# Optimization experiments

Hardware: AMD Instinct MI355X
Metric: run time of the kernel (lower is better)

The kernel has to match this reference:

```python
import jax, jax.numpy as jnp
import numpy as np

N, NTIMES, D_FEAT = 2048, 32, 128


def setup_inputs() -> dict:
    key = jax.random.key(0)
    k1, k2 = jax.random.split(key)
    return {
        "target_fairness": jnp.zeros((), dtype=jnp.float32),
        "prediction": jax.random.uniform(k1, (N, NTIMES), dtype=jnp.float32),
        "X_distance": jax.random.normal(k2, (N, D_FEAT), dtype=jnp.float32),
        "ntimes": NTIMES,
        "scale": jnp.ones((), dtype=jnp.float32),
    }


def reference(target_fairness, prediction, X_distance, ntimes, scale):
    n = prediction.shape[0]
    # cosine distance matrix: 1 - cos_sim, matches sklearn cosine_distances
    norms = jnp.linalg.norm(X_distance, axis=1, keepdims=True)
    Xn = X_distance / norms
    dist = 1.0 - Xn @ Xn.T  # [N, N]
    # pairwise |pred_j - pred_k| over all time points: [N, N, T]
    diff = jnp.abs(prediction[:, None, :] - prediction[None, :, :])
    hinge = jnp.maximum(0.0, diff - scale * dist[:, :, None])
    # only pairs k > j contribute
    mask = jnp.triu(jnp.ones((n, n), dtype=bool), k=1)
    R_beta = jnp.sum(jnp.where(mask[:, :, None], hinge, 0.0))
    model_fairness = 2.0 * R_beta / (n * (n - 1) * ntimes)
    return jnp.maximum(0.0, model_fairness - target_fairness)
```

## Files before the change

### kernel.cpp

```cpp
#include <hip/hip_runtime.h>

#define N 2048
#define T 32
#define D 128
#define BT 32
#define MT (N / BT)
#define NTILES (MT * (MT + 1) / 2)
#define STR 36

typedef float floatx4 __attribute__((ext_vector_type(4)));
typedef short bf16x8 __attribute__((ext_vector_type(8)));

#define LGKM0() __builtin_amdgcn_s_waitcnt(0xc07f)

__device__ __forceinline__ void split8(float4 a, float4 b, bf16x8& h, bf16x8& l) {
  float v[8] = {a.x, a.y, a.z, a.w, b.x, b.y, b.z, b.w};
#pragma unroll
  for (int i = 0; i < 8; ++i) {
    unsigned u = __float_as_uint(v[i]);
    h[i] = (short)(u >> 16);
    float lo = v[i] - __uint_as_float(u & 0xffff0000u);
    l[i] = (short)(__float_as_uint(lo) >> 16);
  }
}

__device__ __forceinline__ float sumsq8(float4 a, float4 b) {
  return a.x * a.x + a.y * a.y + a.z * a.z + a.w * a.w +
         b.x * b.x + b.y * b.y + b.z * b.z + b.w * b.w;
}

__global__ __launch_bounds__(64) void pair_kernel(
    const float* __restrict__ pred,
    const float* __restrict__ X,
    const float* __restrict__ scale_p,
    double* __restrict__ partials) {
  __shared__ float Pa[BT * STR], Pb[BT * STR];
  __shared__ float nrmA[BT], nrmB[BT];

  const int t = blockIdx.x;
  int a = (int)((2 * MT + 1 -
                 sqrtf((float)((2 * MT + 1) * (2 * MT + 1) - 8 * t))) * 0.5f);
  while (a > 0 && t < a * MT - a * (a - 1) / 2) --a;
  while (t >= (a + 1) * MT - (a + 1) * a / 2) ++a;
  const int b = a + (t - (a * MT - a * (a - 1) / 2));

  const int tid  = threadIdx.x;
  const int m    = tid & 15;
  const int quad = tid >> 4;
  const int aRow0 = a * BT, bRow0 = b * BT;
  const float scale = scale_p[0];

  {
    const int srow = tid >> 1, co = (tid & 1) << 4;
    const float* par = pred + (size_t)(aRow0 + srow) * T + co;
    const float* pbr = pred + (size_t)(bRow0 + srow) * T + co;
#pragma unroll
    for (int j = 0; j < 4; ++j) {
      *(float4*)(&Pa[srow * STR + co + 4 * j]) = *(const float4*)(par + 4 * j);
      *(float4*)(&Pb[srow * STR + co + 4 * j]) = *(const float4*)(pbr + 4 * j);
    }
  }

  floatx4 acc[2][2];
#pragma unroll
  for (int I = 0; I < 2; ++I)
#pragma unroll
    for (int J = 0; J < 2; ++J) acc[I][J] = (floatx4){0.f, 0.f, 0.f, 0.f};
  float ssA[2] = {0.f, 0.f}, ssB[2] = {0.f, 0.f};

  const float* xa0 = X + (size_t)(aRow0 + m) * D + quad * 8;
  const float* xb0 = X + (size_t)(bRow0 + m) * D + quad * 8;

#pragma unroll
  for (int ks = 0; ks < 4; ++ks) {
    bf16x8 hA[2], lA[2], hB[2], lB[2];
#pragma unroll
    for (int I = 0; I < 2; ++I) {
      float4 u0 = *(const float4*)(xa0 + (size_t)I * 16 * D + ks * 32);
      float4 u1 = *(const float4*)(xa0 + (size_t)I * 16 * D + ks * 32 + 4);
      ssA[I] += sumsq8(u0, u1);
      split8(u0, u1, hA[I], lA[I]);
      float4 w0 = *(const float4*)(xb0 + (size_t)I * 16 * D + ks * 32);
      float4 w1 = *(const float4*)(xb0 + (size_t)I * 16 * D + ks * 32 + 4);
      ssB[I] += sumsq8(w0, w1);
      split8(w0, w1, hB[I], lB[I]);
    }
#pragma unroll
    for (int I = 0; I < 2; ++I)
#pragma unroll
      for (int J = 0; J < 2; ++J) {
        acc[I][J] = __builtin_amdgcn_mfma_f32_16x16x32_bf16(hA[I], hB[J],
                                                            acc[I][J], 0, 0, 0);
        acc[I][J] = __builtin_amdgcn_mfma_f32_16x16x32_bf16(hA[I], lB[J],
                                                            acc[I][J], 0, 0, 0);
        acc[I][J] = __builtin_amdgcn_mfma_f32_16x16x32_bf16(lA[I], hB[J],
                                                            acc[I][J], 0, 0, 0);
      }
  }

#pragma unroll
  for (int I = 0; I < 2; ++I) {
    ssA[I] += __shfl_xor(ssA[I], 16, 64);
    ssA[I] += __shfl_xor(ssA[I], 32, 64);
    ssB[I] += __shfl_xor(ssB[I], 16, 64);
    ssB[I] += __shfl_xor(ssB[I], 32, 64);
  }
  if (quad == 0) {
#pragma unroll
    for (int I = 0; I < 2; ++I) {
      nrmA[16 * I + m] = rsqrtf(ssA[I]);
      nrmB[16 * I + m] = rsqrtf(ssB[I]);
    }
  }
  LGKM0();

  float na[2][4], nb[2];
#pragma unroll
  for (int I = 0; I < 2; ++I) {
#pragma unroll
    for (int r = 0; r < 4; ++r) na[I][r] = nrmA[16 * I + quad * 4 + r];
    nb[I] = nrmB[16 * I + m];
  }
  float sd[2][2][4], ps[2][2][4];
#pragma unroll
  for (int I = 0; I < 2; ++I)
#pragma unroll
    for (int J = 0; J < 2; ++J)
#pragma unroll
      for (int r = 0; r < 4; ++r) {
        sd[I][J][r] = scale * (1.0f - acc[I][J][r] * na[I][r] * nb[J]);
        ps[I][J][r] = 0.0f;
      }

#pragma unroll
  for (int t4 = 0; t4 < 8; ++t4) {
    float4 qb[2];
    qb[0] = *(const float4*)(&Pb[m * STR + t4 * 4]);
    qb[1] = *(const float4*)(&Pb[(16 + m) * STR + t4 * 4]);
#pragma unroll
    for (int I = 0; I < 2; ++I)
#pragma unroll
      for (int r = 0; r < 4; ++r) {
        float4 qa = *(const float4*)(&Pa[(16 * I + quad * 4 + r) * STR + t4 * 4]);
#pragma unroll
        for (int J = 0; J < 2; ++J) {
          float s = sd[I][J][r];
          ps[I][J][r] += fmaxf(fabsf(qa.x - qb[J].x), s) +
                         fmaxf(fabsf(qa.y - qb[J].y), s) +
                         fmaxf(fabsf(qa.z - qb[J].z), s) +
                         fmaxf(fabsf(qa.w - qb[J].w), s);
        }
      }
  }

  float tsum = 0.0f;
#pragma unroll
  for (int I = 0; I < 2; ++I)
#pragma unroll
    for (int J = 0; J < 2; ++J)
#pragma unroll
      for (int r = 0; r < 4; ++r) {
        int j = aRow0 + 16 * I + quad * 4 + r;
        int k = bRow0 + 16 * J + m;
        tsum += (k > j) ? (ps[I][J][r] - 32.0f * sd[I][J][r]) : 0.0f;
      }

  double dsum = (double)tsum;
#pragma unroll
  for (int off = 32; off > 0; off >>= 1) dsum += __shfl_down(dsum, off, 64);
  if (tid == 0) partials[blockIdx.x] = dsum;
}

__global__ __launch_bounds__(256) void finalize_kernel(
    const double* __restrict__ partials, const float* __restrict__ target,
    float* __restrict__ out) {
  __shared__ double red[4];
  double s = 0.0;
  for (int i = threadIdx.x; i < NTILES; i += 256) s += partials[i];
#pragma unroll
  for (int off = 32; off > 0; off >>= 1) s += __shfl_down(s, off, 64);
  int wave = threadIdx.x >> 6, lane = threadIdx.x & 63;
  if (lane == 0) red[wave] = s;
  __syncthreads();
  if (threadIdx.x == 0) {
    double tot = red[0] + red[1] + red[2] + red[3];
    double mf  = 2.0 * tot / ((double)N * (double)(N - 1) * (double)T);
    double r   = mf - (double)target[0];
    out[0] = (float)(r > 0.0 ? r : 0.0);
  }
}

extern "C" void kernel_launch(void* const* d_in, const int* in_sizes, int n_in,
                              void* d_out, int out_size, void* d_ws, size_t ws_size,
                              hipStream_t stream) {
  const float* target = (const float*)d_in[0];
  const float* pred   = (const float*)d_in[1];
  const float* X      = (const float*)d_in[2];
  const float* scale  = (const float*)d_in[4];

  double* partials = (double*)d_ws;

  pair_kernel<<<dim3(NTILES), dim3(64), 0, stream>>>(pred, X, scale, partials);
  finalize_kernel<<<dim3(1), dim3(256), 0, stream>>>(partials, target,
                                                     (float*)d_out);
}
```

Before: 88.09 us.

## Split fused pair kernel into gram and hinge kernels with time-split tiles

```diff
diff --git a/kernel.cpp b/kernel.cpp
--- a/kernel.cpp
+++ b/kernel.cpp
@@ -6,7 +6,7 @@
 #define BT 32
 #define MT (N / BT)
 #define NTILES (MT * (MT + 1) / 2)
-#define STR 36
+#define PSTR 20
 
 typedef float floatx4 __attribute__((ext_vector_type(4)));
 typedef short bf16x8 __attribute__((ext_vector_type(8)));
@@ -29,37 +29,28 @@
          b.x * b.x + b.y * b.y + b.z * b.z + b.w * b.w;
 }
 
-__global__ __launch_bounds__(64) void pair_kernel(
-    const float* __restrict__ pred,
+__device__ __forceinline__ void tile_decode(int t, int& a, int& b) {
+  a = (int)((2 * MT + 1 -
+             sqrtf((float)((2 * MT + 1) * (2 * MT + 1) - 8 * t))) * 0.5f);
+  while (a > 0 && t < a * MT - a * (a - 1) / 2) --a;
+  while (t >= (a + 1) * MT - (a + 1) * a / 2) ++a;
+  b = a + (t - (a * MT - a * (a - 1) / 2));
+}
+
+__global__ __launch_bounds__(64) void gram_kernel(
     const float* __restrict__ X,
     const float* __restrict__ scale_p,
-    double* __restrict__ partials) {
-  __shared__ float Pa[BT * STR], Pb[BT * STR];
+    float* __restrict__ sd_out) {
   __shared__ float nrmA[BT], nrmB[BT];
 
-  const int t = blockIdx.x;
-  int a = (int)((2 * MT + 1 -
-                 sqrtf((float)((2 * MT + 1) * (2 * MT + 1) - 8 * t))) * 0.5f);
-  while (a > 0 && t < a * MT - a * (a - 1) / 2) --a;
-  while (t >= (a + 1) * MT - (a + 1) * a / 2) ++a;
-  const int b = a + (t - (a * MT - a * (a - 1) / 2));
+  int a, b;
+  tile_decode(blockIdx.x, a, b);
 
   const int tid  = threadIdx.x;
   const int m    = tid & 15;
   const int quad = tid >> 4;
   const int aRow0 = a * BT, bRow0 = b * BT;
   const float scale = scale_p[0];
-
-  {
-    const int srow = tid >> 1, co = (tid & 1) << 4;
-    const float* par = pred + (size_t)(aRow0 + srow) * T + co;
-    const float* pbr = pred + (size_t)(bRow0 + srow) * T + co;
-#pragma unroll
-    for (int j = 0; j < 4; ++j) {
-      *(float4*)(&Pa[srow * STR + co + 4 * j]) = *(const float4*)(par + 4 * j);
-      *(float4*)(&Pb[srow * STR + co + 4 * j]) = *(const float4*)(pbr + 4 * j);
-    }
-  }
 
   floatx4 acc[2][2];
 #pragma unroll
@@ -121,6 +112,44 @@
     for (int r = 0; r < 4; ++r) na[I][r] = nrmA[16 * I + quad * 4 + r];
     nb[I] = nrmB[16 * I + m];
   }
+  float* out = sd_out + (size_t)blockIdx.x * 1024 + tid;
+#pragma unroll
+  for (int I = 0; I < 2; ++I)
+#pragma unroll
+    for (int J = 0; J < 2; ++J)
+#pragma unroll
+      for (int r = 0; r < 4; ++r)
+        out[(I * 8 + J * 4 + r) * 64] =
+            scale * (1.0f - acc[I][J][r] * na[I][r] * nb[J]);
+}
+
+__global__ __launch_bounds__(64) void hinge_kernel(
+    const float* __restrict__ pred,
+    const float* __restrict__ sd_in,
+    double* __restrict__ partials) {
+  __shared__ float Pa[BT * PSTR], Pb[BT * PSTR];
+
+  const int tile = blockIdx.x >> 1;
+  const int th   = blockIdx.x & 1;
+  int a, b;
+  tile_decode(tile, a, b);
+
+  const int tid  = threadIdx.x;
+  const int m    = tid & 15;
+  const int quad = tid >> 4;
+  const int aRow0 = a * BT, bRow0 = b * BT;
+
+  {
+    const int srow = tid >> 1, co = (tid & 1) << 3;
+    const float* par = pred + (size_t)(aRow0 + srow) * T + th * 16 + co;
+    const float* pbr = pred + (size_t)(bRow0 + srow) * T + th * 16 + co;
+    *(float4*)(&Pa[srow * PSTR + co])     = *(const float4*)(par);
+    *(float4*)(&Pa[srow * PSTR + co + 4]) = *(const float4*)(par + 4);
+    *(float4*)(&Pb[srow * PSTR + co])     = *(const float4*)(pbr);
+    *(float4*)(&Pb[srow * PSTR + co + 4]) = *(const float4*)(pbr + 4);
+  }
+
+  const float* sin_ = sd_in + (size_t)tile * 1024 + tid;
   float sd[2][2][4], ps[2][2][4];
 #pragma unroll
   for (int I = 0; I < 2; ++I)
@@ -128,20 +157,21 @@
     for (int J = 0; J < 2; ++J)
 #pragma unroll
       for (int r = 0; r < 4; ++r) {
-        sd[I][J][r] = scale * (1.0f - acc[I][J][r] * na[I][r] * nb[J]);
+        sd[I][J][r] = sin_[(I * 8 + J * 4 + r) * 64];
         ps[I][J][r] = 0.0f;
       }
-
-#pragma unroll
-  for (int t4 = 0; t4 < 8; ++t4) {
+  LGKM0();
+
+#pragma unroll
+  for (int t4 = 0; t4 < 4; ++t4) {
     float4 qb[2];
-    qb[0] = *(const float4*)(&Pb[m * STR + t4 * 4]);
-    qb[1] = *(const float4*)(&Pb[(16 + m) * STR + t4 * 4]);
+    qb[0] = *(const float4*)(&Pb[m * PSTR + t4 * 4]);
+    qb[1] = *(const float4*)(&Pb[(16 + m) * PSTR + t4 * 4]);
 #pragma unroll
     for (int I = 0; I < 2; ++I)
 #pragma unroll
       for (int r = 0; r < 4; ++r) {
-        float4 qa = *(const float4*)(&Pa[(16 * I + quad * 4 + r) * STR + t4 * 4]);
+        float4 qa = *(const float4*)(&Pa[(16 * I + quad * 4 + r) * PSTR + t4 * 4]);
 #pragma unroll
         for (int J = 0; J < 2; ++J) {
           float s = sd[I][J][r];
@@ -162,7 +192,7 @@
       for (int r = 0; r < 4; ++r) {
         int j = aRow0 + 16 * I + quad * 4 + r;
         int k = bRow0 + 16 * J + m;
-        tsum += (k > j) ? (ps[I][J][r] - 32.0f * sd[I][J][r]) : 0.0f;
+        tsum += (k > j) ? (ps[I][J][r] - 16.0f * sd[I][J][r]) : 0.0f;
       }
 
   double dsum = (double)tsum;
@@ -176,7 +206,7 @@
     float* __restrict__ out) {
   __shared__ double red[4];
   double s = 0.0;
-  for (int i = threadIdx.x; i < NTILES; i += 256) s += partials[i];
+  for (int i = threadIdx.x; i < 2 * NTILES; i += 256) s += partials[i];
 #pragma unroll
   for (int off = 32; off > 0; off >>= 1) s += __shfl_down(s, off, 64);
   int wave = threadIdx.x >> 6, lane = threadIdx.x & 63;
@@ -198,9 +228,11 @@
   const float* X      = (const float*)d_in[2];
   const float* scale  = (const float*)d_in[4];
 
-  double* partials = (double*)d_ws;
-
-  pair_kernel<<<dim3(NTILES), dim3(64), 0, stream>>>(pred, X, scale, partials);
+  float*  sd       = (float*)d_ws;
+  double* partials = (double*)((char*)d_ws + (16u << 20));
+
+  gram_kernel<<<dim3(NTILES), dim3(64), 0, stream>>>(X, scale, sd);
+  hinge_kernel<<<dim3(2 * NTILES), dim3(64), 0, stream>>>(pred, sd, partials);
   finalize_kernel<<<dim3(1), dim3(256), 0, stream>>>(partials, target,
                                                      (float*)d_out);
 }
```

Result: slower. 91.41 us (+3.8%).

## Split fused pair kernel into presplit, Gram-matrix, and hinge kernels

Applied to the files above, without the earlier changes.

```diff
diff --git a/kernel.cpp b/kernel.cpp
--- a/kernel.cpp
+++ b/kernel.cpp
@@ -6,43 +6,44 @@
 #define BT 32
 #define MT (N / BT)
 #define NTILES (MT * (MT + 1) / 2)
-#define STR 36
+#define HJ 8
+#define NHBLK 4224
 
 typedef float floatx4 __attribute__((ext_vector_type(4)));
 typedef short bf16x8 __attribute__((ext_vector_type(8)));
 
-#define LGKM0() __builtin_amdgcn_s_waitcnt(0xc07f)
-
-__device__ __forceinline__ void split8(float4 a, float4 b, bf16x8& h, bf16x8& l) {
-  float v[8] = {a.x, a.y, a.z, a.w, b.x, b.y, b.z, b.w};
-#pragma unroll
-  for (int i = 0; i < 8; ++i) {
-    unsigned u = __float_as_uint(v[i]);
-    h[i] = (short)(u >> 16);
-    float lo = v[i] - __uint_as_float(u & 0xffff0000u);
-    l[i] = (short)(__float_as_uint(lo) >> 16);
-  }
+__device__ __forceinline__ void tile_decode(int t, int& a, int& b) {
+  a = (int)((2 * MT + 1 -
+             sqrtf((float)((2 * MT + 1) * (2 * MT + 1) - 8 * t))) * 0.5f);
+  while (a > 0 && t < a * MT - a * (a - 1) / 2) --a;
+  while (t >= (a + 1) * MT - (a + 1) * a / 2) ++a;
+  b = a + (t - (a * MT - a * (a - 1) / 2));
 }
 
-__device__ __forceinline__ float sumsq8(float4 a, float4 b) {
-  return a.x * a.x + a.y * a.y + a.z * a.z + a.w * a.w +
-         b.x * b.x + b.y * b.y + b.z * b.z + b.w * b.w;
+__global__ __launch_bounds__(256) void presplit_kernel(
+    const float* __restrict__ X, unsigned* __restrict__ hX,
+    unsigned* __restrict__ lX) {
+  const int row  = blockIdx.x * 4 + (threadIdx.x >> 6);
+  const int lane = threadIdx.x & 63;
+  float2 v = ((const float2*)(X + (size_t)row * D))[lane];
+  float ss = v.x * v.x + v.y * v.y;
+#pragma unroll
+  for (int off = 32; off > 0; off >>= 1) ss += __shfl_xor(ss, off, 64);
+  const float rn = rsqrtf(ss);
+  const float ax = v.x * rn, ay = v.y * rn;
+  const unsigned ux = __float_as_uint(ax), uy = __float_as_uint(ay);
+  const float lxf = ax - __uint_as_float(ux & 0xffff0000u);
+  const float lyf = ay - __uint_as_float(uy & 0xffff0000u);
+  hX[(size_t)row * 64 + lane] = (ux >> 16) | ((uy >> 16) << 16);
+  lX[(size_t)row * 64 + lane] =
+      (__float_as_uint(lxf) >> 16) | ((__float_as_uint(lyf) >> 16) << 16);
 }
 
-__global__ __launch_bounds__(64) void pair_kernel(
-    const float* __restrict__ pred,
-    const float* __restrict__ X,
-    const float* __restrict__ scale_p,
-    double* __restrict__ partials) {
-  __shared__ float Pa[BT * STR], Pb[BT * STR];
-  __shared__ float nrmA[BT], nrmB[BT];
-
-  const int t = blockIdx.x;
-  int a = (int)((2 * MT + 1 -
-                 sqrtf((float)((2 * MT + 1) * (2 * MT + 1) - 8 * t))) * 0.5f);
-  while (a > 0 && t < a * MT - a * (a - 1) / 2) --a;
-  while (t >= (a + 1) * MT - (a + 1) * a / 2) ++a;
-  const int b = a + (t - (a * MT - a * (a - 1) / 2));
+__global__ __launch_bounds__(64) void gram_kernel(
+    const unsigned short* __restrict__ hX, const unsigned short* __restrict__ lX,
+    const float* __restrict__ scale_p, float* __restrict__ sdm) {
+  int a, b;
+  tile_decode(blockIdx.x, a, b);
 
   const int tid  = threadIdx.x;
   const int m    = tid & 15;
@@ -50,40 +51,26 @@
   const int aRow0 = a * BT, bRow0 = b * BT;
   const float scale = scale_p[0];
 
-  {
-    const int srow = tid >> 1, co = (tid & 1) << 4;
-    const float* par = pred + (size_t)(aRow0 + srow) * T + co;
-    const float* pbr = pred + (size_t)(bRow0 + srow) * T + co;
-#pragma unroll
-    for (int j = 0; j < 4; ++j) {
-      *(float4*)(&Pa[srow * STR + co + 4 * j]) = *(const float4*)(par + 4 * j);
-      *(float4*)(&Pb[srow * STR + co + 4 * j]) = *(const float4*)(pbr + 4 * j);
-    }
-  }
-
   floatx4 acc[2][2];
 #pragma unroll
   for (int I = 0; I < 2; ++I)
 #pragma unroll
     for (int J = 0; J < 2; ++J) acc[I][J] = (floatx4){0.f, 0.f, 0.f, 0.f};
-  float ssA[2] = {0.f, 0.f}, ssB[2] = {0.f, 0.f};
 
-  const float* xa0 = X + (size_t)(aRow0 + m) * D + quad * 8;
-  const float* xb0 = X + (size_t)(bRow0 + m) * D + quad * 8;
+  const unsigned short* ha0 = hX + (size_t)(aRow0 + m) * D + quad * 8;
+  const unsigned short* la0 = lX + (size_t)(aRow0 + m) * D + quad * 8;
+  const unsigned short* hb0 = hX + (size_t)(bRow0 + m) * D + quad * 8;
+  const unsigned short* lb0 = lX + (size_t)(bRow0 + m) * D + quad * 8;
 
 #pragma unroll
   for (int ks = 0; ks < 4; ++ks) {
     bf16x8 hA[2], lA[2], hB[2], lB[2];
 #pragma unroll
     for (int I = 0; I < 2; ++I) {
-      float4 u0 = *(const float4*)(xa0 + (size_t)I * 16 * D + ks * 32);
-      float4 u1 = *(const float4*)(xa0 + (size_t)I * 16 * D + ks * 32 + 4);
-      ssA[I] += sumsq8(u0, u1);
-      split8(u0, u1, hA[I], lA[I]);
-      float4 w0 = *(const float4*)(xb0 + (size_t)I * 16 * D + ks * 32);
-      float4 w1 = *(const float4*)(xb0 + (size_t)I * 16 * D + ks * 32 + 4);
-      ssB[I] += sumsq8(w0, w1);
-      split8(w0, w1, hB[I], lB[I]);
+      hA[I] = *(const bf16x8*)(ha0 + (size_t)I * 16 * D + ks * 32);
+      lA[I] = *(const bf16x8*)(la0 + (size_t)I * 16 * D + ks * 32);
+      hB[I] = *(const bf16x8*)(hb0 + (size_t)I * 16 * D + ks * 32);
+      lB[I] = *(const bf16x8*)(lb0 + (size_t)I * 16 * D + ks * 32);
     }
 #pragma unroll
     for (int I = 0; I < 2; ++I)
@@ -99,76 +86,58 @@
   }
 
 #pragma unroll
-  for (int I = 0; I < 2; ++I) {
-    ssA[I] += __shfl_xor(ssA[I], 16, 64);
-    ssA[I] += __shfl_xor(ssA[I], 32, 64);
-    ssB[I] += __shfl_xor(ssB[I], 16, 64);
-    ssB[I] += __shfl_xor(ssB[I], 32, 64);
-  }
-  if (quad == 0) {
-#pragma unroll
-    for (int I = 0; I < 2; ++I) {
-      nrmA[16 * I + m] = rsqrtf(ssA[I]);
-      nrmB[16 * I + m] = rsqrtf(ssB[I]);
-    }
-  }
-  LGKM0();
-
-  float na[2][4], nb[2];
-#pragma unroll
-  for (int I = 0; I < 2; ++I) {
-#pragma unroll
-    for (int r = 0; r < 4; ++r) na[I][r] = nrmA[16 * I + quad * 4 + r];
-    nb[I] = nrmB[16 * I + m];
-  }
-  float sd[2][2][4], ps[2][2][4];
-#pragma unroll
   for (int I = 0; I < 2; ++I)
 #pragma unroll
     for (int J = 0; J < 2; ++J)
 #pragma unroll
       for (int r = 0; r < 4; ++r) {
-        sd[I][J][r] = scale * (1.0f - acc[I][J][r] * na[I][r] * nb[J]);
-        ps[I][J][r] = 0.0f;
+        const int row = aRow0 + 16 * I + quad * 4 + r;
+        const int col = bRow0 + 16 * J + m;
+        sdm[(size_t)row * N + col] = scale * (1.0f - acc[I][J][r]);
       }
+}
 
+__global__ __launch_bounds__(64) void hinge_kernel(
+    const float* __restrict__ pred, const float* __restrict__ sdm,
+    double* __restrict__ partials) {
+  const int bid = blockIdx.x;
+  int kb = (int)((-1.0f + sqrtf(1.0f + (float)bid)) * 0.5f);
+  while (kb > 0 && 4 * kb * (kb + 1) > bid) --kb;
+  while (4 * (kb + 1) * (kb + 2) <= bid) ++kb;
+  const int jb = bid - 4 * kb * (kb + 1);
+
+  const int lane = threadIdx.x;
+  const int k    = kb * 64 + lane;
+  const int j0   = jb * HJ;
+
+  float4 pb[8];
+  const float4* pk = (const float4*)(pred + (size_t)k * T);
 #pragma unroll
-  for (int t4 = 0; t4 < 8; ++t4) {
-    float4 qb[2];
-    qb[0] = *(const float4*)(&Pb[m * STR + t4 * 4]);
-    qb[1] = *(const float4*)(&Pb[(16 + m) * STR + t4 * 4]);
-#pragma unroll
-    for (int I = 0; I < 2; ++I)
-#pragma unroll
-      for (int r = 0; r < 4; ++r) {
-        float4 qa = *(const float4*)(&Pa[(16 * I + quad * 4 + r) * STR + t4 * 4]);
-#pragma unroll
-        for (int J = 0; J < 2; ++J) {
-          float s = sd[I][J][r];
-          ps[I][J][r] += fmaxf(fabsf(qa.x - qb[J].x), s) +
-                         fmaxf(fabsf(qa.y - qb[J].y), s) +
-                         fmaxf(fabsf(qa.z - qb[J].z), s) +
-                         fmaxf(fabsf(qa.w - qb[J].w), s);
-        }
-      }
-  }
+  for (int q = 0; q < 8; ++q) pb[q] = pk[q];
 
   float tsum = 0.0f;
+#pragma unroll 2
+  for (int jj = 0; jj < HJ; ++jj) {
+    const int j = j0 + jj;
+    const float sdv = sdm[(size_t)j * N + kb * 64 + lane];
+    const float4* pj = (const float4*)(pred + (size_t)j * T);
+    float ps0 = 0.f, ps1 = 0.f, ps2 = 0.f, ps3 = 0.f;
 #pragma unroll
-  for (int I = 0; I < 2; ++I)
-#pragma unroll
-    for (int J = 0; J < 2; ++J)
-#pragma unroll
-      for (int r = 0; r < 4; ++r) {
-        int j = aRow0 + 16 * I + quad * 4 + r;
-        int k = bRow0 + 16 * J + m;
-        tsum += (k > j) ? (ps[I][J][r] - 32.0f * sd[I][J][r]) : 0.0f;
-      }
+    for (int q = 0; q < 8; ++q) {
+      float4 pa = pj[q];
+      ps0 += fmaxf(fabsf(pa.x - pb[q].x), sdv);
+      ps1 += fmaxf(fabsf(pa.y - pb[q].y), sdv);
+      ps2 += fmaxf(fabsf(pa.z - pb[q].z), sdv);
+      ps3 += fmaxf(fabsf(pa.w - pb[q].w), sdv);
+    }
+    const float pss = (ps0 + ps1) + (ps2 + ps3);
+    tsum += (k > j) ? (pss - 32.0f * sdv) : 0.0f;
+  }
 
   double dsum = (double)tsum;
 #pragma unroll
   for (int off = 32; off > 0; off >>= 1) dsum += __shfl_down(dsum, off, 64);
-  if (tid == 0) partials[blockIdx.x] = dsum;
+  if (lane == 0) partials[bid] = dsum;
 }
 
 __global__ __launch_bounds__(256) void finalize_kernel(
@@ -176,7 +145,7 @@
     float* __restrict__ out) {
   __shared__ double red[4];
   double s = 0.0;
-  for (int i = threadIdx.x; i < NTILES; i += 256) s += partials[i];
+  for (int i = threadIdx.x; i < NHBLK; i += 256) s += partials[i];
 #pragma unroll
   for (int off = 32; off > 0; off >>= 1) s += __shfl_down(s, off, 64);
   int wave = threadIdx.x >> 6, lane = threadIdx.x & 63;
@@ -198,9 +167,15 @@
   const float* X      = (const float*)d_in[2];
   const float* scale  = (const float*)d_in[4];
 
-  double* partials = (double*)d_ws;
+  float*    sdm      = (float*)d_ws;
+  unsigned* hX       = (unsigned*)((char*)d_ws + (16u << 20));
+  unsigned* lX       = (unsigned*)((char*)d_ws + (17u << 20));
+  double*   partials = (double*)((char*)d_ws + (18u << 20));
 
-  pair_kernel<<<dim3(NTILES), dim3(64), 0, stream>>>(pred, X, scale, partials);
+  presplit_kernel<<<dim3(N / 4), dim3(256), 0, stream>>>(X, hX, lX);
+  gram_kernel<<<dim3(NTILES), dim3(64), 0, stream>>>(
+      (const unsigned short*)hX, (const unsigned short*)lX, scale, sdm);
+  hinge_kernel<<<dim3(NHBLK), dim3(64), 0, stream>>>(pred, sdm, partials);
   finalize_kernel<<<dim3(1), dim3(256), 0, stream>>>(partials, target,
                                                      (float*)d_out);
 }
```

After: 91.22 us. +3.5%, slower.

## Fuse finalize into pair kernel via atomic last-block reduction; split tiles across waves

Applied to the files above, without the earlier changes.

```diff
diff --git a/kernel.cpp b/kernel.cpp
--- a/kernel.cpp
+++ b/kernel.cpp
@@ -6,7 +6,9 @@
 #define BT 32
 #define MT (N / BT)
 #define NTILES (MT * (MT + 1) / 2)
-#define STR 36
+#define NWAVES (2 * NTILES)
+#define NBLK (NWAVES / 4)
+#define PSTR 33
 
 typedef float floatx4 __attribute__((ext_vector_type(4)));
 typedef short bf16x8 __attribute__((ext_vector_type(8)));
@@ -29,164 +31,157 @@
          b.x * b.x + b.y * b.y + b.z * b.z + b.w * b.w;
 }
 
-__global__ __launch_bounds__(64) void pair_kernel(
+__device__ __forceinline__ void tile_decode(int t, int& a, int& b) {
+  a = (int)((2 * MT + 1 -
+             sqrtf((float)((2 * MT + 1) * (2 * MT + 1) - 8 * t))) * 0.5f);
+  while (a > 0 && t < a * MT - a * (a - 1) / 2) --a;
+  while (t >= (a + 1) * MT - (a + 1) * a / 2) ++a;
+  b = a + (t - (a * MT - a * (a - 1) / 2));
+}
+
+__global__ __launch_bounds__(256) void fused_kernel(
     const float* __restrict__ pred,
     const float* __restrict__ X,
     const float* __restrict__ scale_p,
-    double* __restrict__ partials) {
-  __shared__ float Pa[BT * STR], Pb[BT * STR];
-  __shared__ float nrmA[BT], nrmB[BT];
-
-  const int t = blockIdx.x;
-  int a = (int)((2 * MT + 1 -
-                 sqrtf((float)((2 * MT + 1) * (2 * MT + 1) - 8 * t))) * 0.5f);
-  while (a > 0 && t < a * MT - a * (a - 1) / 2) --a;
-  while (t >= (a + 1) * MT - (a + 1) * a / 2) ++a;
-  const int b = a + (t - (a * MT - a * (a - 1) / 2));
+    const float* __restrict__ target,
+    double* __restrict__ acc,
+    unsigned* __restrict__ counter,
+    float* __restrict__ out) {
+  __shared__ float P[4][48 * PSTR];
+  __shared__ float nrmA[4][16], nrmB[4][32];
+  __shared__ double red[4];
 
   const int tid  = threadIdx.x;
-  const int m    = tid & 15;
-  const int quad = tid >> 4;
+  const int wid  = tid >> 6;
+  const int lane = tid & 63;
+  const int w    = blockIdx.x * 4 + wid;
+  const int tile = w >> 1;
+  const int h    = w & 1;
+
+  int a, b;
+  tile_decode(tile, a, b);
   const int aRow0 = a * BT, bRow0 = b * BT;
+  const int m    = lane & 15;
+  const int quad = lane >> 4;
   const float scale = scale_p[0];
 
-  {
-    const int srow = tid >> 1, co = (tid & 1) << 4;
-    const float* par = pred + (size_t)(aRow0 + srow) * T + co;
-    const float* pbr = pred + (size_t)(bRow0 + srow) * T + co;
-#pragma unroll
-    for (int j = 0; j < 4; ++j) {
-      *(float4*)(&Pa[srow * STR + co + 4 * j]) = *(const float4*)(par + 4 * j);
-      *(float4*)(&Pb[srow * STR + co + 4 * j]) = *(const float4*)(pbr + 4 * j);
-    }
-  }
-
-  floatx4 acc[2][2];
-#pragma unroll
-  for (int I = 0; I < 2; ++I)
-#pragma unroll
-    for (int J = 0; J < 2; ++J) acc[I][J] = (floatx4){0.f, 0.f, 0.f, 0.f};
-  float ssA[2] = {0.f, 0.f}, ssB[2] = {0.f, 0.f};
-
-  const float* xa0 = X + (size_t)(aRow0 + m) * D + quad * 8;
+#pragma unroll
+  for (int s = 0; s < 6; ++s) {
+    const int idx = s * 64 + lane;
+    const int row = idx >> 3;
+    const int fo  = (idx & 7) * 4;
+    const int grow = (row < 16) ? (aRow0 + 16 * h + row) : (bRow0 + row - 16);
+    *(float4*)(&P[wid][row * PSTR + fo]) =
+        *(const float4*)(pred + (size_t)grow * T + fo);
+  }
+
+  floatx4 accf[2];
+  accf[0] = (floatx4){0.f, 0.f, 0.f, 0.f};
+  accf[1] = (floatx4){0.f, 0.f, 0.f, 0.f};
+  float ssA = 0.f, ssB[2] = {0.f, 0.f};
+
+  const float* xar = X + (size_t)(aRow0 + 16 * h + m) * D + quad * 8;
   const float* xb0 = X + (size_t)(bRow0 + m) * D + quad * 8;
 
 #pragma unroll
   for (int ks = 0; ks < 4; ++ks) {
-    bf16x8 hA[2], lA[2], hB[2], lB[2];
-#pragma unroll
-    for (int I = 0; I < 2; ++I) {
-      float4 u0 = *(const float4*)(xa0 + (size_t)I * 16 * D + ks * 32);
-      float4 u1 = *(const float4*)(xa0 + (size_t)I * 16 * D + ks * 32 + 4);
-      ssA[I] += sumsq8(u0, u1);
-      split8(u0, u1, hA[I], lA[I]);
-      float4 w0 = *(const float4*)(xb0 + (size_t)I * 16 * D + ks * 32);
-      float4 w1 = *(const float4*)(xb0 + (size_t)I * 16 * D + ks * 32 + 4);
-      ssB[I] += sumsq8(w0, w1);
-      split8(w0, w1, hB[I], lB[I]);
-    }
-#pragma unroll
-    for (int I = 0; I < 2; ++I)
-#pragma unroll
-      for (int J = 0; J < 2; ++J) {
-        acc[I][J] = __builtin_amdgcn_mfma_f32_16x16x32_bf16(hA[I], hB[J],
-                                                            acc[I][J], 0, 0, 0);
-        acc[I][J] = __builtin_amdgcn_mfma_f32_16x16x32_bf16(hA[I], lB[J],
-                                                            acc[I][J], 0, 0, 0);
-        acc[I][J] = __builtin_amdgcn_mfma_f32_16x16x32_bf16(lA[I], hB[J],
-                                                            acc[I][J], 0, 0, 0);
-      }
-  }
-
-#pragma unroll
-  for (int I = 0; I < 2; ++I) {
-    ssA[I] += __shfl_xor(ssA[I], 16, 64);
-    ssA[I] += __shfl_xor(ssA[I], 32, 64);
-    ssB[I] += __shfl_xor(ssB[I], 16, 64);
-    ssB[I] += __shfl_xor(ssB[I], 32, 64);
+    bf16x8 hA, lA, hB[2], lB[2];
+    {
+      float4 u0 = *(const float4*)(xar + ks * 32);
+      float4 u1 = *(const float4*)(xar + ks * 32 + 4);
+      ssA += sumsq8(u0, u1);
+      split8(u0, u1, hA, lA);
+    }
+#pragma unroll
+    for (int J = 0; J < 2; ++J) {
+      float4 w0 = *(const float4*)(xb0 + (size_t)J * 16 * D + ks * 32);
+      float4 w1 = *(const float4*)(xb0 + (size_t)J * 16 * D + ks * 32 + 4);
+      ssB[J] += sumsq8(w0, w1);
+      split8(w0, w1, hB[J], lB[J]);
+    }
+#pragma unroll
+    for (int J = 0; J < 2; ++J) {
+      accf[J] = __builtin_amdgcn_mfma_f32_16x16x32_bf16(hA, hB[J], accf[J], 0, 0, 0);
+      accf[J] = __builtin_amdgcn_mfma_f32_16x16x32_bf16(hA, lB[J], accf[J], 0, 0, 0);
+      accf[J] = __builtin_amdgcn_mfma_f32_16x16x32_bf16(lA, hB[J], accf[J], 0, 0, 0);
+    }
+  }
+
+  ssA += __shfl_xor(ssA, 16, 64);
+  ssA += __shfl_xor(ssA, 32, 64);
+#pragma unroll
+  for (int J = 0; J < 2; ++J) {
+    ssB[J] += __shfl_xor(ssB[J], 16, 64);
+    ssB[J] += __shfl_xor(ssB[J], 32, 64);
   }
   if (quad == 0) {
-#pragma unroll
-    for (int I = 0; I < 2; ++I) {
-      nrmA[16 * I + m] = rsqrtf(ssA[I]);
-      nrmB[16 * I + m] = rsqrtf(ssB[I]);
-    }
+    nrmA[wid][m] = rsqrtf(ssA);
+    nrmB[wid][m]      = rsqrtf(ssB[0]);
+    nrmB[wid][16 + m] = rsqrtf(ssB[1]);
   }
   LGKM0();
 
-  float na[2][4], nb[2];
-#pragma unroll
-  for (int I = 0; I < 2; ++I) {
-#pragma unroll
-    for (int r = 0; r < 4; ++r) na[I][r] = nrmA[16 * I + quad * 4 + r];
-    nb[I] = nrmB[16 * I + m];
-  }
-  float sd[2][2][4], ps[2][2][4];
-#pragma unroll
-  for (int I = 0; I < 2; ++I)
-#pragma unroll
-    for (int J = 0; J < 2; ++J)
-#pragma unroll
-      for (int r = 0; r < 4; ++r) {
-        sd[I][J][r] = scale * (1.0f - acc[I][J][r] * na[I][r] * nb[J]);
-        ps[I][J][r] = 0.0f;
-      }
+  float na[4], nb[2];
+#pragma unroll
+  for (int r = 0; r < 4; ++r) na[r] = nrmA[wid][quad * 4 + r];
+  nb[0] = nrmB[wid][m];
+  nb[1] = nrmB[wid][16 + m];
+
+  float sd[2][4], ps[2][4];
+#pragma unroll
+  for (int J = 0; J < 2; ++J)
+#pragma unroll
+    for (int r = 0; r < 4; ++r) {
+      sd[J][r] = scale * (1.0f - accf[J][r] * na[r] * nb[J]);
+      ps[J][r] = 0.0f;
+    }
 
 #pragma unroll
   for (int t4 = 0; t4 < 8; ++t4) {
     float4 qb[2];
-    qb[0] = *(const float4*)(&Pb[m * STR + t4 * 4]);
-    qb[1] = *(const float4*)(&Pb[(16 + m) * STR + t4 * 4]);
-#pragma unroll
-    for (int I = 0; I < 2; ++I)
-#pragma unroll
-      for (int r = 0; r < 4; ++r) {
-        float4 qa = *(const float4*)(&Pa[(16 * I + quad * 4 + r) * STR + t4 * 4]);
-#pragma unroll
-        for (int J = 0; J < 2; ++J) {
-          float s = sd[I][J][r];
-          ps[I][J][r] += fmaxf(fabsf(qa.x - qb[J].x), s) +
-                         fmaxf(fabsf(qa.y - qb[J].y), s) +
-                         fmaxf(fabsf(qa.z - qb[J].z), s) +
-                         fmaxf(fabsf(qa.w - qb[J].w), s);
-        }
+    qb[0] = *(const float4*)(&P[wid][(16 + m) * PSTR + t4 * 4]);
+    qb[1] = *(const float4*)(&P[wid][(32 + m) * PSTR + t4 * 4]);
+#pragma unroll
+    for (int r = 0; r < 4; ++r) {
+      float4 qa = *(const float4*)(&P[wid][(quad * 4 + r) * PSTR + t4 * 4]);
+#pragma unroll
+      for (int J = 0; J < 2; ++J) {
+        float s = sd[J][r];
+        ps[J][r] += fmaxf(fabsf(qa.x - qb[J].x), s) +
+                    fmaxf(fabsf(qa.y - qb[J].y), s) +
+                    fmaxf(fabsf(qa.z - qb[J].z), s) +
+                    fmaxf(fabsf(qa.w - qb[J].w), s);
       }
+    }
   }
 
   float tsum = 0.0f;
 #pragma unroll
-  for (int I = 0; I < 2; ++I)
-#pragma unroll
-    for (int J = 0; J < 2; ++J)
-#pragma unroll
-      for (int r = 0; r < 4; ++r) {
-        int j = aRow0 + 16 * I + quad * 4 + r;
-        int k = bRow0 + 16 * J + m;
-        tsum += (k > j) ? (ps[I][J][r] - 32.0f * sd[I][J][r]) : 0.0f;
-      }
+  for (int J = 0; J < 2; ++J)
+#pragma unroll
+    for (int r = 0; r < 4; ++r) {
+      const int ja   = aRow0 + 16 * h + quad * 4 + r;
+      const int kcol = bRow0 + 16 * J + m;
+      tsum += (kcol > ja) ? (ps[J][r] - 32.0f * sd[J][r]) : 0.0f;
+    }
 
   double dsum = (double)tsum;
 #pragma unroll
   for (int off = 32; off > 0; off >>= 1) dsum += __shfl_down(dsum, off, 64);
-  if (tid == 0) partials[blockIdx.x] = dsum;
-}
-
-__global__ __launch_bounds__(256) void finalize_kernel(
-    const double* __restrict__ partials, const float* __restrict__ target,
-    float* __restrict__ out) {
-  __shared__ double red[4];
-  double s = 0.0;
-  for (int i = threadIdx.x; i < NTILES; i += 256) s += partials[i];
-#pragma unroll
-  for (int off = 32; off > 0; off >>= 1) s += __shfl_down(s, off, 64);
-  int wave = threadIdx.x >> 6, lane = threadIdx.x & 63;
-  if (lane == 0) red[wave] = s;
+  if (lane == 0) red[wid] = dsum;
   __syncthreads();
-  if (threadIdx.x == 0) {
-    double tot = red[0] + red[1] + red[2] + red[3];
-    double mf  = 2.0 * tot / ((double)N * (double)(N - 1) * (double)T);
-    double r   = mf - (double)target[0];
-    out[0] = (float)(r > 0.0 ? r : 0.0);
+
+  if (tid == 0) {
+    const double blksum = red[0] + red[1] + red[2] + red[3];
+    atomicAdd(acc, blksum);
+    __threadfence();
+    const unsigned done = atomicAdd(counter, 1u);
+    if (done == NBLK - 1) {
+      const double tot = atomicAdd(acc, 0.0);
+      const double mf  = 2.0 * tot / ((double)N * (double)(N - 1) * (double)T);
+      const double r   = mf - (double)target[0];
+      out[0] = (float)(r > 0.0 ? r : 0.0);
+    }
   }
 }
 
@@ -198,9 +193,10 @@
   const float* X      = (const float*)d_in[2];
   const float* scale  = (const float*)d_in[4];
 
-  double* partials = (double*)d_ws;
-
-  pair_kernel<<<dim3(NTILES), dim3(64), 0, stream>>>(pred, X, scale, partials);
-  finalize_kernel<<<dim3(1), dim3(256), 0, stream>>>(partials, target,
-                                                     (float*)d_out);
-}
+  double*   acc     = (double*)d_ws;
+  unsigned* counter = (unsigned*)((char*)d_ws + 8);
+
+  hipMemsetAsync(d_ws, 0, 16, stream);
+  fused_kernel<<<dim3(NBLK), dim3(256), 0, stream>>>(
+      pred, X, scale, target, acc, counter, (float*)d_out);
+}
```

Result: slower. 103.4 us (+17.3%).
